# Kernel optimization log

Measured on AMD Instinct MI355X. Metric: run time of the kernel, lower is better.

The kernel has to match this reference:

```python
import jax, jax.numpy as jnp
import numpy as np

B, C, D, H, W = 2, 384, 32, 32, 32
HEADS, WS = 12, 5
HD = C // HEADS
PAD = WS // 2
SCALE = HD ** -0.5


def setup_inputs() -> dict:
    key = jax.random.key(0)
    ks = jax.random.split(key, 6)
    return {
        "x": jax.random.normal(ks[0], (B, C, D, H, W), jnp.float32),
        "w_qkv": jax.random.normal(ks[1], (3 * C, C), jnp.float32) * 0.02,
        "b_qkv": jax.random.normal(ks[2], (3 * C,), jnp.float32) * 0.02,
        "w_proj": jax.random.normal(ks[3], (C, C), jnp.float32) * 0.02,
        "b_proj": jax.random.normal(ks[4], (C,), jnp.float32) * 0.02,
        "pos_embed": jax.random.normal(ks[5], (HD, WS, WS, WS), jnp.float32) * 0.02,
    }


def reference(x, w_qkv, b_qkv, w_proj, b_proj, pos_embed):
    # 1x1x1 conv == pointwise linear over channels
    qkv = jnp.einsum('bcdhw,oc->bodhw', x, w_qkv) + b_qkv[None, :, None, None, None]
    q, k, v = jnp.split(qkv, 3, axis=1)
    q = q.reshape(B, HEADS, HD, D, H, W)
    k = k.reshape(B, HEADS, HD, D, H, W)
    v = v.reshape(B, HEADS, HD, D, H, W)
    pad_cfg = ((0, 0), (0, 0), (0, 0), (PAD, PAD), (PAD, PAD), (PAD, PAD))
    k_pad = jnp.pad(k, pad_cfg)  # zero padding, as in torch F.pad(value=0)
    v_pad = jnp.pad(v, pad_cfg)
    # per-offset scores: equivalent to unfold(ws)^3 without materializing windows
    scores = []
    for dz in range(WS):
        for dy in range(WS):
            for dx in range(WS):
                k_s = k_pad[:, :, :, dz:dz + D, dy:dy + H, dx:dx + W]
                # pos embed is added to k windows (including padded zeros) as in original
                k_s = k_s + pos_embed[:, dz, dy, dx][None, None, :, None, None, None]
                scores.append(jnp.sum(q * k_s, axis=2) * SCALE)  # [B,heads,D,H,W]
    scores = jnp.stack(scores, axis=-1)  # [B,heads,D,H,W,WS^3]
    wts = jax.nn.softmax(scores, axis=-1)
    out = jnp.zeros((B, HEADS, HD, D, H, W), x.dtype)
    i = 0
    for dz in range(WS):
        for dy in range(WS):
            for dx in range(WS):
                v_s = v_pad[:, :, :, dz:dz + D, dy:dy + H, dx:dx + W]
                out = out + wts[..., i][:, :, None] * v_s
                i += 1
    out = out.reshape(B, C, D, H, W)
    out = jnp.einsum('bcdhw,oc->bodhw', out, w_proj) + b_proj[None, :, None, None, None]
    return out
```

## Files before the change

### kernel.cpp

```cpp
#include <hip/hip_runtime.h>


#define NB 2
#define NC 384
#define NHEADS 12
#define NHD 32
#define NS 32768
#define PERB 12582912
#define SCALE_F 0.17677669529663687f
#define LOG2E_F 1.4426950408889634f
#define SL_F (0.17677669529663687f * 1.4426950408889634f)

typedef unsigned short bfr;
typedef float floatx4 __attribute__((ext_vector_type(4)));
typedef float f32x4 __attribute__((ext_vector_type(4)));
typedef short bf16x8 __attribute__((ext_vector_type(8)));
typedef short short4v __attribute__((ext_vector_type(4)));

union B8 { floatx4 v; bfr h[8]; };

__device__ __forceinline__ float b2f(bfr u) {
    union { unsigned int i; float f; } v;
    v.i = (unsigned int)u << 16;
    return v.f;
}
__device__ __forceinline__ bfr f2b(float f) {
    union { float f; unsigned int i; } v;
    v.f = f;
    unsigned int x = v.i;
    return (bfr)((x + 0x7fffu + ((x >> 16) & 1u)) >> 16);
}
__device__ __forceinline__ unsigned cvt_pk2(float lo, float hi) {
    unsigned r;
    asm("v_cvt_pk_bf16_f32 %0, %1, %2" : "=v"(r) : "v"(lo), "v"(hi));
    return r;
}

__global__ void fill_code(float* out, float code) {
    for (size_t i = (size_t)blockIdx.x*256 + threadIdx.x; i < (size_t)NB*PERB;
         i += (size_t)gridDim.x*256) out[i] = code;
}

__global__ __launch_bounds__(256) void xpose(
    const float* __restrict__ x, bfr* __restrict__ xT, int b)
{
    __shared__ __attribute__((aligned(16))) bfr tl[256][40];
    const int tid = threadIdx.x;
    const int s0  = blockIdx.x * 256;
    for (int c0 = 0; c0 < NC; c0 += 32) {
        if (c0) __syncthreads();
        const int c  = tid >> 3;
        const int sb = (tid & 7) * 4;
        #pragma unroll
        for (int j = 0; j < 8; ++j) {
            const int s4 = sb + j*32;
            floatx4 v =
                *(const floatx4*)&x[((size_t)b*NC + c0 + c)*NS + s0 + s4];
            #pragma unroll
            for (int i = 0; i < 4; ++i) tl[s4 + i][c] = f2b(v[i]);
        }
        __syncthreads();
        floatx4* dst = (floatx4*)&xT[(size_t)(s0 + tid)*NC + c0];
        #pragma unroll
        for (int q = 0; q < 4; ++q)
            dst[q] = *(const floatx4*)&tl[tid][q*8];
    }
}

__global__ __launch_bounds__(256) void qkv_mfma(
    const bfr* __restrict__ xT, const float* __restrict__ w,
    const float* __restrict__ bias,
    bfr* __restrict__ qT, bfr* __restrict__ kT, bfr* __restrict__ vT)
{
    __shared__ __attribute__((aligned(16))) bfr wl[128*40];
    __shared__ __attribute__((aligned(16))) bfr xl[128*40];
    __shared__ float bsh[128];
    const int tid  = threadIdx.x;
    const int lane = tid & 63;
    const int wave = tid >> 6;
    const int wo   = (wave & 1) * 64;
    const int wsq  = (wave >> 1) * 64;
    const int s0   = blockIdx.y * 128;
    const int o0   = blockIdx.x * 128;
    const int m16  = lane & 15;
    const int g    = lane >> 4;

    if (tid < 128) bsh[tid] = bias[o0 + tid];

    f32x4 acc[4][4];
    #pragma unroll
    for (int i = 0; i < 4; ++i)
        #pragma unroll
        for (int j = 0; j < 4; ++j) acc[i][j] = (f32x4){0.f, 0.f, 0.f, 0.f};

    for (int kc = 0; kc < 12; ++kc) {
        const int c0 = kc * 32;
        #pragma unroll
        for (int r = 0; r < 4; ++r) {
            const int idx = r*256 + tid;
            const int o   = idx >> 3;
            const int c4  = (idx & 7) * 4;
            floatx4 wv = *(const floatx4*)&w[(size_t)(o0 + o)*NC + c0 + c4];
            *(uint2*)&wl[o*40 + c4] =
                make_uint2(cvt_pk2(wv[0], wv[1]), cvt_pk2(wv[2], wv[3]));
        }
        #pragma unroll
        for (int r = 0; r < 2; ++r) {
            const int idx = r*256 + tid;
            const int s   = idx >> 2;
            const int gg  = idx & 3;
            *(floatx4*)&xl[s*40 + gg*8] =
                *(const floatx4*)&xT[(size_t)(s0 + s)*NC + c0 + gg*8];
        }
        __syncthreads();
        bf16x8 af[4], bfg[4];
        #pragma unroll
        for (int i = 0; i < 4; ++i)
            af[i] = *(bf16x8*)&wl[(wo + i*16 + m16)*40 + g*8];
        #pragma unroll
        for (int j = 0; j < 4; ++j)
            bfg[j] = *(bf16x8*)&xl[(wsq + j*16 + m16)*40 + g*8];
        #pragma unroll
        for (int i = 0; i < 4; ++i)
            #pragma unroll
            for (int j = 0; j < 4; ++j)
                acc[i][j] = __builtin_amdgcn_mfma_f32_16x16x32_bf16(
                    af[i], bfg[j], acc[i][j], 0, 0, 0);
        __syncthreads();
    }

    const int tens = blockIdx.x / 3;
    bfr* dstT = (tens == 0) ? qT : ((tens == 1) ? kT : vT);
    const int remb = o0 - tens*NC;
    const int q4   = g * 4;
    #pragma unroll
    for (int i = 0; i < 4; ++i) {
        const int olb = wo + i*16 + q4;
        const int ob  = remb + olb;
        const int hh  = ob >> 5;
        const int cc  = ob & 31;
        #pragma unroll
        for (int j = 0; j < 4; ++j) {
            const int s = s0 + wsq + j*16 + m16;
            const unsigned u0 = cvt_pk2(acc[i][j][0] + bsh[olb + 0],
                                        acc[i][j][1] + bsh[olb + 1]);
            const unsigned u1 = cvt_pk2(acc[i][j][2] + bsh[olb + 2],
                                        acc[i][j][3] + bsh[olb + 3]);
            *(uint2*)&dstT[((size_t)hh*NS + s)*NHD + cc] = make_uint2(u0, u1);
        }
    }
}

__global__ __launch_bounds__(256, 4) void attn3d(
    const bfr* __restrict__ qT, const bfr* __restrict__ kT,
    const bfr* __restrict__ vT, const float* __restrict__ pe,
    bfr* __restrict__ aT)
{
    __shared__ __attribute__((aligned(16))) unsigned char smem[40960];
    bfr (*kl)[40]   = reinterpret_cast<bfr(*)[40]>(smem);
    bfr (*vtl)[136] = reinterpret_cast<bfr(*)[136]>(smem + 10240);
    bfr (*pel)[40]  = reinterpret_cast<bfr(*)[40]>(smem);
    bfr (*ql)[40]   = reinterpret_cast<bfr(*)[40]>(smem + 18944);
    bfr (*qpl)[132] = reinterpret_cast<bfr(*)[132]>(smem + 24064);

    const int tid  = threadIdx.x;
    const int lane = tid & 63;
    const int wave = tid >> 6;
    const int m16  = lane & 15;
    const int g    = lane >> 4;
    const int g4   = g << 2;
    const int bx   = blockIdx.x;
    const int tz = bx >> 6, ty = (bx >> 3) & 7, tx = bx & 7;
    const size_t hb = (size_t)blockIdx.y * NS;

    {
        const int qr = tid >> 2, part = tid & 3;
        const int qzr = qr >> 4, qyr = (qr >> 2) & 3, qxr = qr & 3;
        const size_t sq =
            (size_t)(tz*4 + qzr)*1024 + (ty*4 + qyr)*32 + (tx*4 + qxr);
        *(floatx4*)&ql[qr][part*8] =
            *(const floatx4*)&qT[(hb + sq)*NHD + part*8];
    }
    for (int e = tid; e < 4000; e += 256) {
        const int hd = e / 125;
        const int n  = e - hd*125;
        pel[n][hd] = f2b(pe[e]);
    }
    if (tid < 96) pel[125 + (tid >> 5)][tid & 31] = 0;
    __syncthreads();

    const int wq = wave*16 + m16;
    const bf16x8 bq = *(const bf16x8*)&ql[wq][g*8];

    #pragma unroll
    for (int t = 0; t < 8; ++t) {
        bf16x8 pa = *(const bf16x8*)&pel[t*16 + m16][g*8];
        f32x4 qa = __builtin_amdgcn_mfma_f32_16x16x32_bf16(
            pa, bq, (f32x4){0.f, 0.f, 0.f, 0.f}, 0, 0, 0);
        const unsigned w0 = cvt_pk2(qa[0]*SL_F, qa[1]*SL_F);
        const unsigned w1 = cvt_pk2(qa[2]*SL_F, qa[3]*SL_F);
        *(uint2*)&qpl[wq][t*16 + g4] = make_uint2(w0, w1);
    }
    if (g == 0) qpl[wq][128] = 0xFF80u;

    const int qy = m16 >> 2, qx = m16 & 3;
    unsigned nopk[4];
    #pragma unroll
    for (int tt = 0; tt < 4; ++tt) {
        unsigned v = 0;
        #pragma unroll
        for (int r = 0; r < 4; ++r) {
            const int t0 = g4 + r;
            const int hy = 2*tt + (t0 >> 3), hx = t0 & 7;
            const int dy = hy - qy, dx = hx - qx;
            const bool ok = ((unsigned)dy < 5u) && ((unsigned)dx < 5u);
            v |= (unsigned)(ok ? (dy*5 + dx) : 128) << (8*r);
        }
        nopk[tt] = v;
    }
    const bfr* qprow = qpl[wq];
    const int a0 = (m16 + 32*(g & 1)) * 4;
    const int a1 = a0 + 64;
    const bool ghi = (g >= 2);

    float m = -1e30f, l = 0.f;
    f32x4 o[2];
    o[0] = (f32x4){0.f, 0.f, 0.f, 0.f};
    o[1] = (f32x4){0.f, 0.f, 0.f, 0.f};

    for (int c = 0; c < 4; ++c) {
        __syncthreads();
        #pragma unroll
        for (int r2 = 0; r2 < 2; ++r2) {
            const int idx = r2*256 + tid;
            const int key = idx >> 2, part = idx & 3;
            const int hz = key >> 6, hy = (key >> 3) & 7, hx = key & 7;
            const int gz = tz*4 - 2 + 2*c + hz, gy = ty*4 - 2 + hy,
                      gx = tx*4 - 2 + hx;
            floatx4 kv = (floatx4){0.f, 0.f, 0.f, 0.f};
            if ((unsigned)gz < 32u && (unsigned)gy < 32u && (unsigned)gx < 32u)
                kv = *(const floatx4*)
                     &kT[(hb + gz*1024 + gy*32 + gx)*NHD + part*8];
            *(floatx4*)&kl[key][part*8] = kv;
        }
        {
            const int kp = tid & 63, hdo = tid >> 6;
            const int aK = 2*kp;
            const int hz = aK >> 6;
            const int hy = (aK >> 3) & 7, hx = aK & 7;
            const int gz = tz*4 - 2 + 2*c + hz, gy = ty*4 - 2 + hy,
                      gx = tx*4 - 2 + hx;
            const bool vzy = ((unsigned)gz < 32u) && ((unsigned)gy < 32u);
            B8 va, vb;
            va.v = (floatx4){0.f, 0.f, 0.f, 0.f};
            vb.v = (floatx4){0.f, 0.f, 0.f, 0.f};
            const size_t gb = hb + gz*1024 + gy*32;
            if (vzy && (unsigned)gx < 32u)
                va.v = *(const floatx4*)&vT[(gb + gx)*NHD + hdo*8];
            if (vzy && (unsigned)(gx + 1) < 32u)
                vb.v = *(const floatx4*)&vT[(gb + gx + 1)*NHD + hdo*8];
            #pragma unroll
            for (int i = 0; i < 8; ++i) {
                const unsigned u = (unsigned)va.h[i] | ((unsigned)vb.h[i] << 16);
                *(unsigned*)&vtl[hdo*8 + i][aK] = u;
            }
        }
        __syncthreads();

        #pragma unroll
        for (int zl = 0; zl < 2; ++zl) {
            const int dz = 2*c + zl - wave;
            if ((unsigned)dz > 4u) continue;
            const int nz = dz * 25;
            f32x4 s[4];
            __builtin_amdgcn_s_setprio(1);
            #pragma unroll
            for (int tt = 0; tt < 4; ++tt) {
                bf16x8 ka = *(const bf16x8*)&kl[zl*64 + tt*16 + m16][g*8];
                s[tt] = __builtin_amdgcn_mfma_f32_16x16x32_bf16(
                    ka, bq, (f32x4){0.f, 0.f, 0.f, 0.f}, 0, 0, 0);
            }
            __builtin_amdgcn_s_setprio(0);
            float mx = -1e30f;
            #pragma unroll
            for (int tt = 0; tt < 4; ++tt) {
                #pragma unroll
                for (int r = 0; r < 4; ++r) {
                    const unsigned n =
                        min((unsigned)nz + ((nopk[tt] >> (8*r)) & 255u), 128u);
                    const float qb  = b2f(qprow[n]);
                    const float val = fmaf(s[tt][r], SL_F, qb);
                    s[tt][r] = val;
                    mx = fmaxf(mx, val);
                }
            }
            mx = fmaxf(mx, __shfl_xor(mx, 16));
            mx = fmaxf(mx, __shfl_xor(mx, 32));
            const float mn = fmaxf(m, mx);
            if (__any(mx > m)) {
                const float al = exp2f(m - mn);
                l *= al;
                #pragma unroll
                for (int i = 0; i < 4; ++i) { o[0][i] *= al; o[1][i] *= al; }
                m = mn;
            }
            float ls = 0.f;
            unsigned pk[4][2];
            #pragma unroll
            for (int tt = 0; tt < 4; ++tt) {
                const float p0 = exp2f(s[tt][0] - m);
                const float p1 = exp2f(s[tt][1] - m);
                const float p2 = exp2f(s[tt][2] - m);
                const float p3 = exp2f(s[tt][3] - m);
                ls += (p0 + p1) + (p2 + p3);
                pk[tt][0] = cvt_pk2(p0, p1);
                pk[tt][1] = cvt_pk2(p2, p3);
            }
            ls += __shfl_xor(ls, 16);
            ls += __shfl_xor(ls, 32);
            l += ls;
            #pragma unroll
            for (int ksl = 0; ksl < 2; ++ksl) {
                union { unsigned u[4]; bf16x8 v; } pb;
                #pragma unroll
                for (int w = 0; w < 4; ++w) {
                    const int ad = (w < 2) ? a0 : a1;
                    const int wi = w & 1;
                    const int lo = __builtin_amdgcn_ds_bpermute(
                        ad, (int)pk[2*ksl][wi]);
                    const int hi = __builtin_amdgcn_ds_bpermute(
                        ad, (int)pk[2*ksl + 1][wi]);
                    pb.u[w] = ghi ? (unsigned)hi : (unsigned)lo;
                }
                __builtin_amdgcn_s_setprio(1);
                #pragma unroll
                for (int mt = 0; mt < 2; ++mt) {
                    bf16x8 va = *(const bf16x8*)
                        &vtl[mt*16 + m16][zl*64 + ksl*32 + g*8];
                    o[mt] = __builtin_amdgcn_mfma_f32_16x16x32_bf16(
                        va, pb.v, o[mt], 0, 0, 0);
                }
                __builtin_amdgcn_s_setprio(0);
            }
        }
    }

    const float rl = 1.f / l;
    const size_t sq = (size_t)(tz*4 + wave)*1024 + (ty*4 + qy)*32 + (tx*4 + qx);
    #pragma unroll
    for (int mt = 0; mt < 2; ++mt) {
        const unsigned w0 = cvt_pk2(o[mt][0]*rl, o[mt][1]*rl);
        const unsigned w1 = cvt_pk2(o[mt][2]*rl, o[mt][3]*rl);
        *(uint2*)&aT[(hb + sq)*NHD + mt*16 + g4] = make_uint2(w0, w1);
    }
}

__global__ __launch_bounds__(256) void proj_mfma(
    const bfr* __restrict__ aT, const float* __restrict__ w,
    const float* __restrict__ bias, float* __restrict__ out)
{
    __shared__ __attribute__((aligned(16))) bfr wl[128*40];
    __shared__ __attribute__((aligned(16))) bfr xl[128*40];
    __shared__ float bsh[128];
    const int tid  = threadIdx.x;
    const int lane = tid & 63;
    const int wave = tid >> 6;
    const int wo   = (wave & 1) * 64;
    const int wsq  = (wave >> 1) * 64;
    const int s0   = blockIdx.y * 128;
    const int o0   = blockIdx.x * 128;
    const int m16  = lane & 15;
    const int g    = lane >> 4;

    if (tid < 128) bsh[tid] = bias[o0 + tid];

    f32x4 acc[4][4];
    #pragma unroll
    for (int i = 0; i < 4; ++i)
        #pragma unroll
        for (int j = 0; j < 4; ++j) acc[i][j] = (f32x4){0.f, 0.f, 0.f, 0.f};

    for (int kc = 0; kc < 12; ++kc) {
        const int c0 = kc * 32;
        #pragma unroll
        for (int r = 0; r < 4; ++r) {
            const int idx = r*256 + tid;
            const int o   = idx >> 3;
            const int c4  = (idx & 7) * 4;
            floatx4 wv = *(const floatx4*)&w[(size_t)(o0 + o)*NC + c0 + c4];
            *(uint2*)&wl[o*40 + c4] =
                make_uint2(cvt_pk2(wv[0], wv[1]), cvt_pk2(wv[2], wv[3]));
        }
        #pragma unroll
        for (int r = 0; r < 2; ++r) {
            const int idx = r*256 + tid;
            const int s   = idx >> 2;
            const int gg  = idx & 3;
            *(floatx4*)&xl[s*40 + gg*8] =
                *(const floatx4*)&aT[((size_t)kc*NS + s0 + s)*NHD + gg*8];
        }
        __syncthreads();
        bf16x8 af[4], bfg[4];
        #pragma unroll
        for (int i = 0; i < 4; ++i)
            af[i] = *(bf16x8*)&wl[(wo + i*16 + m16)*40 + g*8];
        #pragma unroll
        for (int j = 0; j < 4; ++j)
            bfg[j] = *(bf16x8*)&xl[(wsq + j*16 + m16)*40 + g*8];
        #pragma unroll
        for (int i = 0; i < 4; ++i)
            #pragma unroll
            for (int j = 0; j < 4; ++j)
                acc[i][j] = __builtin_amdgcn_mfma_f32_16x16x32_bf16(
                    af[i], bfg[j], acc[i][j], 0, 0, 0);
        __syncthreads();
    }

    const int q4 = g * 4;
    #pragma unroll
    for (int i = 0; i < 4; ++i) {
        const int olb = wo + i*16 + q4;
        #pragma unroll
        for (int j = 0; j < 4; ++j) {
            const int s = s0 + wsq + j*16 + m16;
            #pragma unroll
            for (int r = 0; r < 4; ++r)
                out[(size_t)(o0 + olb + r)*NS + s] = acc[i][j][r] + bsh[olb + r];
        }
    }
}

extern "C" void kernel_launch(void* const* d_in, const int* in_sizes, int n_in,
                              void* d_out, int out_size, void* d_ws, size_t ws_size,
                              hipStream_t stream)
{
    const float* x      = (const float*)d_in[0];
    const float* w_qkv  = (const float*)d_in[1];
    const float* b_qkv  = (const float*)d_in[2];
    const float* w_proj = (const float*)d_in[3];
    const float* b_proj = (const float*)d_in[4];
    const float* pe     = (const float*)d_in[5];
    float* outp = (float*)d_out;

    const size_t NEED = (size_t)2 * PERB * sizeof(bfr);
    if (ws_size < NEED) {
        fill_code<<<2048, 256, 0, stream>>>(outp, (float)(ws_size >> 20));
        return;
    }

    bfr* qT = (bfr*)d_ws;
    bfr* vT = qT + PERB;
    bfr* xT = (bfr*)(outp + PERB);
    bfr* kT = xT + (size_t)PERB;

    for (int b = 0; b < NB; ++b) {
        bfr* aT = qT;
        xpose<<<dim3(128, 1, 1), 256, 0, stream>>>(x, xT, b);
        qkv_mfma<<<dim3(9, 256, 1), 256, 0, stream>>>(
            xT, w_qkv, b_qkv, qT, kT, vT);
        attn3d<<<dim3(512, 12, 1), 256, 0, stream>>>(qT, kT, vT, pe, aT);
        proj_mfma<<<dim3(3, 256, 1), 256, 0, stream>>>(
            aT, w_proj, b_proj, outp + (size_t)b * PERB);
    }
}
```

Before: 615.2 us.

## Use padded 3D q-pos-bias table to replace per-element gather index math

Stores the per-query q·pos_embed bias in a padded 5x9x5 layout pre-filled with -inf, so each group of four score elements reads four contiguous entries from one precomputed base offset instead of decoding packed per-element indices with clamping. It also hoists the K/V global-load address and bounds computations out of the chunk loop, and loads both K z-slices per thread directly. Shared memory grows and the launch bound drops from 4 to 3 blocks per CU, which may lower occupancy.

New measurement: 699.2 us. 1.14x slower.

```diff
diff --git a/kernel.cpp b/kernel.cpp
--- a/kernel.cpp
+++ b/kernel.cpp
@@ -151,17 +151,19 @@
     }
 }
 
-__global__ __launch_bounds__(256, 4) void attn3d(
+#define QPL3_OFF 18944
+#define QPL3_ROW 228
+__global__ __launch_bounds__(256, 3) void attn3d(
     const bfr* __restrict__ qT, const bfr* __restrict__ kT,
     const bfr* __restrict__ vT, const float* __restrict__ pe,
     bfr* __restrict__ aT)
 {
-    __shared__ __attribute__((aligned(16))) unsigned char smem[40960];
+    __shared__ __attribute__((aligned(16))) unsigned char smem[48128];
     bfr (*kl)[40]   = reinterpret_cast<bfr(*)[40]>(smem);
     bfr (*vtl)[136] = reinterpret_cast<bfr(*)[136]>(smem + 10240);
     bfr (*pel)[40]  = reinterpret_cast<bfr(*)[40]>(smem);
-    bfr (*ql)[40]   = reinterpret_cast<bfr(*)[40]>(smem + 18944);
-    bfr (*qpl)[132] = reinterpret_cast<bfr(*)[132]>(smem + 24064);
+    bfr (*ql)[40]   = reinterpret_cast<bfr(*)[40]>(smem + 10240);
+    bfr* qpl3       = reinterpret_cast<bfr*>(smem + QPL3_OFF);
 
     const int tid  = threadIdx.x;
     const int lane = tid & 63;
@@ -187,82 +189,96 @@
         pel[n][hd] = f2b(pe[e]);
     }
     if (tid < 96) pel[125 + (tid >> 5)][tid & 31] = 0;
+    {
+        const unsigned p = 0xFF80FF80u;
+        for (int off = tid*16; off < 64*QPL3_ROW*2; off += 256*16)
+            *(uint4*)(smem + QPL3_OFF + off) = make_uint4(p, p, p, p);
+    }
     __syncthreads();
 
     const int wq = wave*16 + m16;
     const bf16x8 bq = *(const bf16x8*)&ql[wq][g*8];
+    bfr* qrow3 = qpl3 + wq*QPL3_ROW;
 
     #pragma unroll
     for (int t = 0; t < 8; ++t) {
         bf16x8 pa = *(const bf16x8*)&pel[t*16 + m16][g*8];
         f32x4 qa = __builtin_amdgcn_mfma_f32_16x16x32_bf16(
             pa, bq, (f32x4){0.f, 0.f, 0.f, 0.f}, 0, 0, 0);
-        const unsigned w0 = cvt_pk2(qa[0]*SL_F, qa[1]*SL_F);
-        const unsigned w1 = cvt_pk2(qa[2]*SL_F, qa[3]*SL_F);
-        *(uint2*)&qpl[wq][t*16 + g4] = make_uint2(w0, w1);
-    }
-    if (g == 0) qpl[wq][128] = 0xFF80u;
+        #pragma unroll
+        for (int r = 0; r < 4; ++r) {
+            const int n = t*16 + g4 + r;
+            if (n < 125) {
+                const int dz  = n / 25, rem = n - dz*25;
+                const int dy  = rem / 5, dx = rem - dy*5;
+                qrow3[dz*45 + dy*9 + 4 + dx] =
+                    (bfr)cvt_pk2(qa[r]*SL_F, qa[r]*SL_F);
+            }
+        }
+    }
 
     const int qy = m16 >> 2, qx = m16 & 3;
-    unsigned nopk[4];
+    const int hb_  = g >> 1;
+    const int xoff = (g & 1)*4 - qx;
+    int pre[4];
     #pragma unroll
     for (int tt = 0; tt < 4; ++tt) {
-        unsigned v = 0;
-        #pragma unroll
-        for (int r = 0; r < 4; ++r) {
-            const int t0 = g4 + r;
-            const int hy = 2*tt + (t0 >> 3), hx = t0 & 7;
-            const int dy = hy - qy, dx = hx - qx;
-            const bool ok = ((unsigned)dy < 5u) && ((unsigned)dx < 5u);
-            v |= (unsigned)(ok ? (dy*5 + dx) : 128) << (8*r);
-        }
-        nopk[tt] = v;
-    }
-    const bfr* qprow = qpl[wq];
+        const int dy = 2*tt + hb_ - qy;
+        pre[tt] = ((unsigned)dy < 5u) ? (dy*9 + 4 + xoff) : 0;
+    }
     const int a0 = (m16 + 32*(g & 1)) * 4;
     const int a1 = a0 + 64;
     const bool ghi = (g >= 2);
+
+    const int gz0 = tz*4 - 2;
+    const int kkey = tid >> 2, kpart = tid & 3;
+    const int kgy  = ty*4 - 2 + ((kkey >> 3) & 7);
+    const int kgx  = tx*4 - 2 + (kkey & 7);
+    const bool kyx = ((unsigned)kgy < 32u) & ((unsigned)kgx < 32u);
+    const int kbase = (int)hb*NHD + (gz0*1024 + kgy*32 + kgx)*NHD + kpart*8;
+    const int vkp = tid & 63, vhdo = tid >> 6;
+    const int vaK = 2*vkp;
+    const int vhz = vaK >> 6;
+    const int vgy = ty*4 - 2 + ((vaK >> 3) & 7);
+    const int vgxa = tx*4 - 2 + (vaK & 7);
+    const bool vya  = ((unsigned)vgy < 32u);
+    const bool voka = vya & ((unsigned)vgxa < 32u);
+    const bool vokb = vya & ((unsigned)(vgxa + 1) < 32u);
+    const int vzb = gz0 + vhz;
+    const int vbase = (int)hb*NHD + (vzb*1024 + vgy*32 + vgxa)*NHD + vhdo*8;
 
     float m = -1e30f, l = 0.f;
     f32x4 o[2];
     o[0] = (f32x4){0.f, 0.f, 0.f, 0.f};
     o[1] = (f32x4){0.f, 0.f, 0.f, 0.f};
+    const floatx4 z4 = (floatx4){0.f, 0.f, 0.f, 0.f};
 
     for (int c = 0; c < 4; ++c) {
         __syncthreads();
-        #pragma unroll
-        for (int r2 = 0; r2 < 2; ++r2) {
-            const int idx = r2*256 + tid;
-            const int key = idx >> 2, part = idx & 3;
-            const int hz = key >> 6, hy = (key >> 3) & 7, hx = key & 7;
-            const int gz = tz*4 - 2 + 2*c + hz, gy = ty*4 - 2 + hy,
-                      gx = tx*4 - 2 + hx;
-            floatx4 kv = (floatx4){0.f, 0.f, 0.f, 0.f};
-            if ((unsigned)gz < 32u && (unsigned)gy < 32u && (unsigned)gx < 32u)
-                kv = *(const floatx4*)
-                     &kT[(hb + gz*1024 + gy*32 + gx)*NHD + part*8];
-            *(floatx4*)&kl[key][part*8] = kv;
-        }
         {
-            const int kp = tid & 63, hdo = tid >> 6;
-            const int aK = 2*kp;
-            const int hz = aK >> 6;
-            const int hy = (aK >> 3) & 7, hx = aK & 7;
-            const int gz = tz*4 - 2 + 2*c + hz, gy = ty*4 - 2 + hy,
-                      gx = tx*4 - 2 + hx;
-            const bool vzy = ((unsigned)gz < 32u) && ((unsigned)gy < 32u);
+            const int kgz  = gz0 + 2*c;
+            const int kidx = kbase + c*65536;
+            floatx4 kv0 = z4, kv1 = z4;
+            if (kyx && (unsigned)kgz < 32u)
+                kv0 = *(const floatx4*)&kT[kidx];
+            if (kyx && (unsigned)(kgz + 1) < 32u)
+                kv1 = *(const floatx4*)&kT[kidx + 32768];
+            *(floatx4*)&kl[kkey][kpart*8] = kv0;
+            *(floatx4*)&kl[kkey + 64][kpart*8] = kv1;
+        }
+        {
+            const int vgz  = vzb + 2*c;
+            const int vidx = vbase + c*65536;
             B8 va, vb;
-            va.v = (floatx4){0.f, 0.f, 0.f, 0.f};
-            vb.v = (floatx4){0.f, 0.f, 0.f, 0.f};
-            const size_t gb = hb + gz*1024 + gy*32;
-            if (vzy && (unsigned)gx < 32u)
-                va.v = *(const floatx4*)&vT[(gb + gx)*NHD + hdo*8];
-            if (vzy && (unsigned)(gx + 1) < 32u)
-                vb.v = *(const floatx4*)&vT[(gb + gx + 1)*NHD + hdo*8];
+            va.v = z4; vb.v = z4;
+            if (voka && (unsigned)vgz < 32u)
+                va.v = *(const floatx4*)&vT[vidx];
+            if (vokb && (unsigned)vgz < 32u)
+                vb.v = *(const floatx4*)&vT[vidx + NHD];
             #pragma unroll
             for (int i = 0; i < 8; ++i) {
                 const unsigned u = (unsigned)va.h[i] | ((unsigned)vb.h[i] << 16);
-                *(unsigned*)&vtl[hdo*8 + i][aK] = u;
+                *(unsigned*)&vtl[vhdo*8 + i][vaK] = u;
             }
         }
         __syncthreads();
@@ -271,7 +287,7 @@
         for (int zl = 0; zl < 2; ++zl) {
             const int dz = 2*c + zl - wave;
             if ((unsigned)dz > 4u) continue;
-            const int nz = dz * 25;
+            const bfr* qz3 = qrow3 + dz*45;
             f32x4 s[4];
             __builtin_amdgcn_s_setprio(1);
             #pragma unroll
@@ -284,15 +300,13 @@
             float mx = -1e30f;
             #pragma unroll
             for (int tt = 0; tt < 4; ++tt) {
-                #pragma unroll
-                for (int r = 0; r < 4; ++r) {
-                    const unsigned n =
-                        min((unsigned)nz + ((nopk[tt] >> (8*r)) & 255u), 128u);
-                    const float qb  = b2f(qprow[n]);
-                    const float val = fmaf(s[tt][r], SL_F, qb);
-                    s[tt][r] = val;
-                    mx = fmaxf(mx, val);
-                }
+                const bfr* p = qz3 + pre[tt];
+                const float v0 = fmaf(s[tt][0], SL_F, b2f(p[0]));
+                const float v1 = fmaf(s[tt][1], SL_F, b2f(p[1]));
+                const float v2 = fmaf(s[tt][2], SL_F, b2f(p[2]));
+                const float v3 = fmaf(s[tt][3], SL_F, b2f(p[3]));
+                s[tt][0] = v0; s[tt][1] = v1; s[tt][2] = v2; s[tt][3] = v3;
+                mx = fmaxf(fmaxf(fmaxf(v0, v1), fmaxf(v2, v3)), mx);
             }
             mx = fmaxf(mx, __shfl_xor(mx, 16));
             mx = fmaxf(mx, __shfl_xor(mx, 32));
```
